# Performance work log

Hardware: AMD Instinct MI355X
Metric: run time of the kernel (lower is better)

The kernel has to match this reference:

```python
import jax, jax.numpy as jnp
import numpy as np

N_NODES = 100_000
E_TOTAL = 1_100_000
# up_scale_edge_ranges: static metadata on the Data object -> baked as constants
EXCLUDE_RANGES = [(1_000_000, 1_100_000)]
_mask = np.ones(E_TOTAL, dtype=bool)
for _s, _e in EXCLUDE_RANGES:
    _mask[_s:_e] = False
KEEP_IDX = np.nonzero(_mask)[0]  # static, shape [1_000_000]


def _mlp(h, w1, b1, w2, b2):
    return jax.nn.relu(h @ w1 + b1) @ w2 + b2


def setup_inputs() -> dict:
    key = jax.random.key(0)
    ks = jax.random.split(key, 12)
    s = 0.05
    return {
        "x": jax.random.normal(ks[0], (N_NODES, 7), dtype=jnp.float32),
        "pos": jax.random.normal(ks[1], (N_NODES, 3), dtype=jnp.float32),
        "edge_index": jax.random.randint(ks[2], (2, E_TOTAL), 0, N_NODES, dtype=jnp.int64),
        "nw1": jax.random.normal(ks[3], (7, 128), dtype=jnp.float32) * s,
        "nb1": jnp.zeros((128,), dtype=jnp.float32),
        "nw2": jax.random.normal(ks[4], (128, 128), dtype=jnp.float32) * s,
        "nb2": jnp.zeros((128,), dtype=jnp.float32),
        "ew1": jax.random.normal(ks[5], (3, 128), dtype=jnp.float32) * s,
        "eb1": jnp.zeros((128,), dtype=jnp.float32),
        "ew2": jax.random.normal(ks[6], (128, 128), dtype=jnp.float32) * s,
        "eb2": jnp.zeros((128,), dtype=jnp.float32),
    }


def reference(x, pos, edge_index, nw1, nb1, nw2, nb2, ew1, eb1, ew2, eb2):
    # static mask over edge ranges (shapes fixed at trace time)
    edges = edge_index[:, KEEP_IDX]                       # [2, E_kept]
    d = pos[edges[0], :2] - pos[edges[1], :2]             # [E_kept, 2]
    norm = jnp.linalg.norm(d, axis=1, keepdims=True)      # [E_kept, 1]
    edges_attr = jnp.concatenate([d, norm], axis=1)       # [E_kept, 3]
    edge_embedding = _mlp(edges_attr, ew1, eb1, ew2, eb2) # [E_kept, 128]
    node_embedding = _mlp(x, nw1, nb1, nw2, nb2)          # [N, 128]
    return (node_embedding, edge_embedding)
```

## Files before the change

### kernel.cpp

```cpp
#include <hip/hip_runtime.h>

typedef short short8 __attribute__((ext_vector_type(8)));
typedef float f32x4 __attribute__((ext_vector_type(4)));
typedef unsigned int u32x2 __attribute__((ext_vector_type(2)));
typedef unsigned int u32x4 __attribute__((ext_vector_type(4)));

#define N_NODES   100000
#define E_KEEP    1000000
#define E_TOTAL_N 1100000
#define EDGE_OUT_BASE 12800000L

#define H1_STRIDE 272
#define STG_STRIDE 272

__device__ __forceinline__ unsigned short f2bf(float f) {
  unsigned int u = __builtin_bit_cast(unsigned int, f);
  u += 0x7fffu + ((u >> 16) & 1u);
  return (unsigned short)(u >> 16);
}

__device__ __forceinline__ unsigned int pack2relu(float lo, float hi) {
  return (unsigned int)f2bf(fmaxf(lo, 0.f)) |
         ((unsigned int)f2bf(fmaxf(hi, 0.f)) << 16);
}
__device__ __forceinline__ unsigned int pack2(float lo, float hi) {
  return (unsigned int)f2bf(lo) | ((unsigned int)f2bf(hi) << 16);
}

__global__ void transpose_w2(const float* __restrict__ nw2,
                             const float* __restrict__ ew2,
                             unsigned short* __restrict__ ws) {
  int idx = blockIdx.x * 256 + threadIdx.x;
  for (int i = idx; i < 32768; i += 8192) {
    int m = i >> 14;
    int w = i & 16383;
    int k = w >> 7;
    int n = w & 127;
    const float* src = m ? ew2 : nw2;
    ws[m * 16384 + n * 128 + k] = f2bf(src[w]);
  }
}

struct SmemLayout {
  float w1f[7 * 128];
  float b1f[128];
  float b2f[128];
  float attr[256 * 7];
  char  h1[2][32 * H1_STRIDE];
  char  stg[32 * STG_STRIDE];
};

template<bool IS_EDGE>
__device__ __forceinline__ void run_path(
    const float* __restrict__ src,
    const int* __restrict__ ei,
    const float* __restrict__ w1,
    const float* __restrict__ b1,
    const float* __restrict__ b2,
    const unsigned short* __restrict__ w2t,
    float* __restrict__ outp, long out_base, int row_limit,
    int bid, SmemLayout& sm)
{
  constexpr int NA = IS_EDGE ? 3 : 7;
  const int t = threadIdx.x;

  if (t < 128) { sm.b1f[t] = b1[t]; sm.b2f[t] = b2[t]; }
  for (int i = t; i < NA * 128; i += 256) sm.w1f[i] = w1[i];

  {
    int r  = bid * 256 + t;
    int rl = r < row_limit ? r : row_limit - 1;
    if (IS_EDGE) {
      int si = ei[rl];
      int di = ei[E_TOTAL_N + rl];
      float ax = src[si * 3]     - src[di * 3];
      float ay = src[si * 3 + 1] - src[di * 3 + 1];
      sm.attr[t * 3 + 0] = ax;
      sm.attr[t * 3 + 1] = ay;
      sm.attr[t * 3 + 2] = sqrtf(ax * ax + ay * ay);
    } else {
#pragma unroll
      for (int cc = 0; cc < 7; ++cc) sm.attr[t * 7 + cc] = src[rl * 7 + cc];
    }
  }

  const int lane = t & 63;
  const int wid  = t >> 6;
  const int rg   = wid & 1;
  const int wc   = wid >> 1;
  const int c    = lane & 15;
  const int g    = lane >> 4;

  short8 wfrag[4][4];
#pragma unroll
  for (int nf = 0; nf < 4; ++nf)
#pragma unroll
    for (int kk = 0; kk < 4; ++kk)
      wfrag[nf][kk] = *(const short8*)(w2t + (wc * 64 + nf * 16 + c) * 128 + kk * 32 + g * 8);

  __syncthreads();

  const int brow = t & 31;
  const int kc   = t >> 5;
  const int k0   = kc * 16;

  const int rrow = rg * 16 + c;

  f32x4 b2v[4];
#pragma unroll
  for (int nf = 0; nf < 4; ++nf)
    b2v[nf] = *(const f32x4*)&sm.b2f[wc * 64 + nf * 16 + g * 4];

  for (int s = 0; s < 8; ++s) {
    char* h1 = sm.h1[s & 1];

    {
      float a[NA];
#pragma unroll
      for (int cc = 0; cc < NA; ++cc) a[cc] = sm.attr[(s * 32 + brow) * NA + cc];

      f32x4 h0 = *(const f32x4*)&sm.b1f[k0];
      f32x4 h1v = *(const f32x4*)&sm.b1f[k0 + 4];
      f32x4 h2 = *(const f32x4*)&sm.b1f[k0 + 8];
      f32x4 h3 = *(const f32x4*)&sm.b1f[k0 + 12];
#pragma unroll
      for (int cc = 0; cc < NA; ++cc) {
        h0  += a[cc] * *(const f32x4*)&sm.w1f[cc * 128 + k0];
        h1v += a[cc] * *(const f32x4*)&sm.w1f[cc * 128 + k0 + 4];
        h2  += a[cc] * *(const f32x4*)&sm.w1f[cc * 128 + k0 + 8];
        h3  += a[cc] * *(const f32x4*)&sm.w1f[cc * 128 + k0 + 12];
      }
      u32x4 dA, dB;
      dA[0] = pack2relu(h0[0], h0[1]);  dA[1] = pack2relu(h0[2], h0[3]);
      dA[2] = pack2relu(h1v[0], h1v[1]); dA[3] = pack2relu(h1v[2], h1v[3]);
      dB[0] = pack2relu(h2[0], h2[1]);  dB[1] = pack2relu(h2[2], h2[3]);
      dB[2] = pack2relu(h3[0], h3[1]);  dB[3] = pack2relu(h3[2], h3[3]);

      char* wp = h1 + brow * H1_STRIDE + kc * 32;
      *(u32x4*)(wp)      = dA;
      *(u32x4*)(wp + 16) = dB;
    }

    __syncthreads();

    {
      f32x4 acc0 = {}, acc1 = {}, acc2 = {}, acc3 = {};
#pragma unroll
      for (int kk = 0; kk < 4; ++kk) {
        short8 hf = *(const short8*)(h1 + rrow * H1_STRIDE + kk * 64 + g * 16);
        acc0 = __builtin_amdgcn_mfma_f32_16x16x32_bf16(wfrag[0][kk], hf, acc0, 0, 0, 0);
        acc1 = __builtin_amdgcn_mfma_f32_16x16x32_bf16(wfrag[1][kk], hf, acc1, 0, 0, 0);
        acc2 = __builtin_amdgcn_mfma_f32_16x16x32_bf16(wfrag[2][kk], hf, acc2, 0, 0, 0);
        acc3 = __builtin_amdgcn_mfma_f32_16x16x32_bf16(wfrag[3][kk], hf, acc3, 0, 0, 0);
      }
      f32x4 av[4] = {acc0 + b2v[0], acc1 + b2v[1], acc2 + b2v[2], acc3 + b2v[3]};
      char* wp = sm.stg + rrow * STG_STRIDE + (wc * 64 + g * 4) * 2;
#pragma unroll
      for (int nf = 0; nf < 4; ++nf) {
        u32x2 d;
        d[0] = pack2(av[nf][0], av[nf][1]);
        d[1] = pack2(av[nf][2], av[nf][3]);
        *(u32x2*)(wp + nf * 32) = d;
      }
    }

    __syncthreads();

    {
      int r0 = bid * 256 + s * 32;
#pragma unroll
      for (int p = 0; p < 2; ++p) {
        int u   = p * 256 + t;
        int row = u >> 4;
        int k16 = u & 15;
        if (r0 + row < row_limit) {
          short8 v = *(const short8*)(sm.stg + row * STG_STRIDE + k16 * 16);
          f32x4 lo, hi;
#pragma unroll
          for (int j = 0; j < 4; ++j) {
            lo[j] = __builtin_bit_cast(float, ((unsigned int)(unsigned short)v[j]) << 16);
            hi[j] = __builtin_bit_cast(float, ((unsigned int)(unsigned short)v[4 + j]) << 16);
          }
          float* op = outp + out_base + (long)(r0 + row) * 128 + k16 * 8;
          *(f32x4*)op       = lo;
          *(f32x4*)(op + 4) = hi;
        }
      }
    }
  }
}

__global__ __launch_bounds__(256, 3) void encoder_kernel(
    const float* __restrict__ x,
    const float* __restrict__ pos,
    const int* __restrict__ ei,
    const float* __restrict__ nw1,
    const float* __restrict__ nb1,
    const float* __restrict__ nb2,
    const float* __restrict__ ew1,
    const float* __restrict__ eb1,
    const float* __restrict__ eb2,
    const unsigned short* __restrict__ ws,
    float* __restrict__ outp,
    int nodeBlocks)
{
  __shared__ SmemLayout sm;
  int bid = blockIdx.x;
  if (bid < nodeBlocks) {
    run_path<false>(x, nullptr, nw1, nb1, nb2, ws, outp, 0L, N_NODES, bid, sm);
  } else {
    run_path<true>(pos, ei, ew1, eb1, eb2, ws + 16384, outp, EDGE_OUT_BASE,
                   E_KEEP, bid - nodeBlocks, sm);
  }
}

extern "C" void kernel_launch(void* const* d_in, const int* in_sizes, int n_in,
                              void* d_out, int out_size, void* d_ws, size_t ws_size,
                              hipStream_t stream) {
  const float* x   = (const float*)d_in[0];
  const float* pos = (const float*)d_in[1];
  const int*   ei  = (const int*)d_in[2];
  const float* nw1 = (const float*)d_in[3];
  const float* nb1 = (const float*)d_in[4];
  const float* nw2 = (const float*)d_in[5];
  const float* nb2 = (const float*)d_in[6];
  const float* ew1 = (const float*)d_in[7];
  const float* eb1 = (const float*)d_in[8];
  const float* ew2 = (const float*)d_in[9];
  const float* eb2 = (const float*)d_in[10];
  unsigned short* ws   = (unsigned short*)d_ws;
  float*          outp = (float*)d_out;

  transpose_w2<<<32, 256, 0, stream>>>(nw2, ew2, ws);

  int nodeBlocks = (N_NODES + 255) / 256;
  int edgeBlocks = (E_KEEP + 255) / 256;
  encoder_kernel<<<nodeBlocks + edgeBlocks, 256, 0, stream>>>(
      x, pos, ei, nw1, nb1, nb2, ew1, eb1, eb2, ws, outp, nodeBlocks);
}
```

Before: 170.0 us.

## Compute layer-1 activations directly in MFMA B-fragment registers, drop h1 LDS staging

Each wave now computes the first-layer hidden activations for its own MFMA operand rows in registers and feeds them straight into the bf16 MFMAs, removing the h1 LDS buffer, its writes and reads, and one barrier per sub-tile. The output staging buffer is double-buffered so the remaining barrier suffices, bf16 packing uses the hardware v_cvt_pk_bf16_f32 instruction, and launch bounds are raised to 4 blocks per CU. The cost is redundant layer-1 work: every wave pair sharing rows recomputes the same hidden values, and register pressure rises under the tighter occupancy target.

```diff
diff --git a/kernel.cpp b/kernel.cpp
--- a/kernel.cpp
+++ b/kernel.cpp
@@ -10,7 +10,6 @@
 #define E_TOTAL_N 1100000
 #define EDGE_OUT_BASE 12800000L
 
-#define H1_STRIDE 272
 #define STG_STRIDE 272
 
 __device__ __forceinline__ unsigned short f2bf(float f) {
@@ -19,12 +18,13 @@
   return (unsigned short)(u >> 16);
 }
 
+__device__ __forceinline__ unsigned int cvtpk(float lo, float hi) {
+  unsigned int r;
+  asm("v_cvt_pk_bf16_f32 %0, %1, %2" : "=v"(r) : "v"(lo), "v"(hi));
+  return r;
+}
 __device__ __forceinline__ unsigned int pack2relu(float lo, float hi) {
-  return (unsigned int)f2bf(fmaxf(lo, 0.f)) |
-         ((unsigned int)f2bf(fmaxf(hi, 0.f)) << 16);
-}
-__device__ __forceinline__ unsigned int pack2(float lo, float hi) {
-  return (unsigned int)f2bf(lo) | ((unsigned int)f2bf(hi) << 16);
+  return cvtpk(fmaxf(lo, 0.f), fmaxf(hi, 0.f));
 }
 
 __global__ void transpose_w2(const float* __restrict__ nw2,
@@ -46,8 +46,7 @@
   float b1f[128];
   float b2f[128];
   float attr[256 * 7];
-  char  h1[2][32 * H1_STRIDE];
-  char  stg[32 * STG_STRIDE];
+  char  stg[2][32 * STG_STRIDE];
 };
 
 template<bool IS_EDGE>
@@ -98,13 +97,9 @@
     for (int kk = 0; kk < 4; ++kk)
       wfrag[nf][kk] = *(const short8*)(w2t + (wc * 64 + nf * 16 + c) * 128 + kk * 32 + g * 8);
 
+  const int rrow = rg * 16 + c;
+
   __syncthreads();
-
-  const int brow = t & 31;
-  const int kc   = t >> 5;
-  const int k0   = kc * 16;
-
-  const int rrow = rg * 16 + c;
 
   f32x4 b2v[4];
 #pragma unroll
@@ -112,54 +107,42 @@
     b2v[nf] = *(const f32x4*)&sm.b2f[wc * 64 + nf * 16 + g * 4];
 
   for (int s = 0; s < 8; ++s) {
-    char* h1 = sm.h1[s & 1];
-
     {
       float a[NA];
 #pragma unroll
-      for (int cc = 0; cc < NA; ++cc) a[cc] = sm.attr[(s * 32 + brow) * NA + cc];
-
-      f32x4 h0 = *(const f32x4*)&sm.b1f[k0];
-      f32x4 h1v = *(const f32x4*)&sm.b1f[k0 + 4];
-      f32x4 h2 = *(const f32x4*)&sm.b1f[k0 + 8];
-      f32x4 h3 = *(const f32x4*)&sm.b1f[k0 + 12];
-#pragma unroll
-      for (int cc = 0; cc < NA; ++cc) {
-        h0  += a[cc] * *(const f32x4*)&sm.w1f[cc * 128 + k0];
-        h1v += a[cc] * *(const f32x4*)&sm.w1f[cc * 128 + k0 + 4];
-        h2  += a[cc] * *(const f32x4*)&sm.w1f[cc * 128 + k0 + 8];
-        h3  += a[cc] * *(const f32x4*)&sm.w1f[cc * 128 + k0 + 12];
-      }
-      u32x4 dA, dB;
-      dA[0] = pack2relu(h0[0], h0[1]);  dA[1] = pack2relu(h0[2], h0[3]);
-      dA[2] = pack2relu(h1v[0], h1v[1]); dA[3] = pack2relu(h1v[2], h1v[3]);
-      dB[0] = pack2relu(h2[0], h2[1]);  dB[1] = pack2relu(h2[2], h2[3]);
-      dB[2] = pack2relu(h3[0], h3[1]);  dB[3] = pack2relu(h3[2], h3[3]);
-
-      char* wp = h1 + brow * H1_STRIDE + kc * 32;
-      *(u32x4*)(wp)      = dA;
-      *(u32x4*)(wp + 16) = dB;
-    }
-
-    __syncthreads();
-
-    {
+      for (int cc = 0; cc < NA; ++cc)
+        a[cc] = sm.attr[(s * 32 + rrow) * NA + cc];
+
       f32x4 acc0 = {}, acc1 = {}, acc2 = {}, acc3 = {};
 #pragma unroll
       for (int kk = 0; kk < 4; ++kk) {
-        short8 hf = *(const short8*)(h1 + rrow * H1_STRIDE + kk * 64 + g * 16);
+        int k0g = kk * 32 + g * 8;
+        f32x4 h0 = *(const f32x4*)&sm.b1f[k0g];
+        f32x4 h1v = *(const f32x4*)&sm.b1f[k0g + 4];
+#pragma unroll
+        for (int cc = 0; cc < NA; ++cc) {
+          h0  += a[cc] * *(const f32x4*)&sm.w1f[cc * 128 + k0g];
+          h1v += a[cc] * *(const f32x4*)&sm.w1f[cc * 128 + k0g + 4];
+        }
+        u32x4 hv;
+        hv[0] = pack2relu(h0[0], h0[1]);
+        hv[1] = pack2relu(h0[2], h0[3]);
+        hv[2] = pack2relu(h1v[0], h1v[1]);
+        hv[3] = pack2relu(h1v[2], h1v[3]);
+        short8 hf = __builtin_bit_cast(short8, hv);
         acc0 = __builtin_amdgcn_mfma_f32_16x16x32_bf16(wfrag[0][kk], hf, acc0, 0, 0, 0);
         acc1 = __builtin_amdgcn_mfma_f32_16x16x32_bf16(wfrag[1][kk], hf, acc1, 0, 0, 0);
         acc2 = __builtin_amdgcn_mfma_f32_16x16x32_bf16(wfrag[2][kk], hf, acc2, 0, 0, 0);
         acc3 = __builtin_amdgcn_mfma_f32_16x16x32_bf16(wfrag[3][kk], hf, acc3, 0, 0, 0);
       }
+
+      char* wp = sm.stg[s & 1] + rrow * STG_STRIDE + (wc * 64 + g * 4) * 2;
       f32x4 av[4] = {acc0 + b2v[0], acc1 + b2v[1], acc2 + b2v[2], acc3 + b2v[3]};
-      char* wp = sm.stg + rrow * STG_STRIDE + (wc * 64 + g * 4) * 2;
 #pragma unroll
       for (int nf = 0; nf < 4; ++nf) {
         u32x2 d;
-        d[0] = pack2(av[nf][0], av[nf][1]);
-        d[1] = pack2(av[nf][2], av[nf][3]);
+        d[0] = cvtpk(av[nf][0], av[nf][1]);
+        d[1] = cvtpk(av[nf][2], av[nf][3]);
         *(u32x2*)(wp + nf * 32) = d;
       }
     }
@@ -167,6 +150,7 @@
     __syncthreads();
 
     {
+      const char* stg = sm.stg[s & 1];
       int r0 = bid * 256 + s * 32;
 #pragma unroll
       for (int p = 0; p < 2; ++p) {
@@ -174,7 +158,7 @@
         int row = u >> 4;
         int k16 = u & 15;
         if (r0 + row < row_limit) {
-          short8 v = *(const short8*)(sm.stg + row * STG_STRIDE + k16 * 16);
+          short8 v = *(const short8*)(stg + row * STG_STRIDE + k16 * 16);
           f32x4 lo, hi;
 #pragma unroll
           for (int j = 0; j < 4; ++j) {
@@ -190,7 +174,7 @@
   }
 }
 
-__global__ __launch_bounds__(256, 3) void encoder_kernel(
+__global__ __launch_bounds__(256, 4) void encoder_kernel(
     const float* __restrict__ x,
     const float* __restrict__ pos,
     const int* __restrict__ ei,
```

Result: no change. 172.4 us (+1.4%).
